# Kernel optimization log

Hardware: AMD Instinct MI355X
Metric: run time of the kernel (lower is better)

The kernel has to match this reference:

```python
import jax, jax.numpy as jnp
import numpy as np

H = 512

def _lstm_cell(x, h, c, Wih, Whh, bih, bhh):
    # PyTorch LSTMCell: gates ordered i, f, g, o
    g = x @ Wih.T + bih + h @ Whh.T + bhh
    i, f, gg, o = jnp.split(g, 4, axis=-1)
    i = jax.nn.sigmoid(i)
    f = jax.nn.sigmoid(f)
    gg = jnp.tanh(gg)
    o = jax.nn.sigmoid(o)
    c_new = f * c + i * gg
    h_new = o * jnp.tanh(c_new)
    return h_new, c_new


def setup_inputs() -> dict:
    key = jax.random.key(0)
    ks = jax.random.split(key, 12)
    B, T = 16, 6574
    s1 = 1.0 / np.sqrt(H)
    u = lambda k, shape: jax.random.uniform(k, shape, jnp.float32, -s1, s1)
    return {
        "input": jax.random.normal(ks[0], (B, T, 2), jnp.float32),
        "W_ih1": u(ks[1], (4 * H, 2)),
        "W_hh1": u(ks[2], (4 * H, H)),
        "b_ih1": u(ks[3], (4 * H,)),
        "b_hh1": u(ks[4], (4 * H,)),
        "W_ih2": u(ks[5], (4 * H, H)),
        "W_hh2": u(ks[6], (4 * H, H)),
        "b_ih2": u(ks[7], (4 * H,)),
        "b_hh2": u(ks[8], (4 * H,)),
        "W_out": u(ks[9], (1, H)),
        "b_out": u(ks[10], (1,)),
    }


def reference(input, W_ih1, W_hh1, b_ih1, b_hh1, W_ih2, W_hh2, b_ih2, b_hh2, W_out, b_out):
    B = input.shape[0]
    h1 = jnp.zeros((B, H), input.dtype)
    c1 = jnp.zeros((B, H), input.dtype)
    h2 = jnp.zeros((B, H), input.dtype)
    c2 = jnp.zeros((B, H), input.dtype)

    def step(carry, x_t):
        h1, c1, h2, c2 = carry
        h1, c1 = _lstm_cell(x_t, h1, c1, W_ih1, W_hh1, b_ih1, b_hh1)
        h2, c2 = _lstm_cell(h1, h2, c2, W_ih2, W_hh2, b_ih2, b_hh2)
        out_t = h2 @ W_out.T + b_out  # [B, 1]
        return (h1, c1, h2, c2), out_t

    xs = jnp.swapaxes(input, 0, 1)  # [T, B, 2]
    _, outs = jax.lax.scan(step, (h1, c1, h2, c2), xs)
    return jnp.swapaxes(outs, 0, 1)  # [B, T, 1]
```

## Files before the change

kernel.cpp:

```cpp
#include <hip/hip_runtime.h>
#include <math.h>

#define NWG  256
#define NTHR 256
#define AGT __HIP_MEMORY_SCOPE_AGENT

#define O_W2  0
#define O_W1  16384
#define O_U   24576
#define O_WX  33280
#define O_B1  33312
#define O_B2  33328
#define O_WO  33344
#define O_XS  33348
#define O_G1  33364
#define O_G2  33492
#define O_C1  33620
#define O_C2  33652
#define O_HN  33684
#define LDS_FLOATS 33720

union U64F2 { unsigned long long u; float f[2]; };

__global__ void ws_init_kernel(unsigned* flags, float* h1g, float* h2g) {
    int i = blockIdx.x * blockDim.x + threadIdx.x;
    int n = gridDim.x * blockDim.x;
    for (int j = i; j < NWG; j += n) flags[j] = 0u;
    for (int j = i; j < 16384; j += n) { h1g[j] = 0.0f; h2g[j] = 0.0f; }
}

__device__ __forceinline__ float sigm(float x) { return 1.0f / (1.0f + __expf(-x)); }
__device__ __forceinline__ float tanh_fast(float x) { return 2.0f / (1.0f + __expf(-2.0f * x)) - 1.0f; }

__device__ __forceinline__ void gbar(unsigned* flags, int wg, int tid, unsigned ph) {
    __syncthreads();
    asm volatile("s_waitcnt vmcnt(0)" ::: "memory");
    if (tid == 0)
        __hip_atomic_store(&flags[wg], ph, __ATOMIC_RELAXED, AGT);
    if (tid < 64) {
        const unsigned long long* f64 = (const unsigned long long*)flags;
        bool done;
        do {
            unsigned long long v0 = __hip_atomic_load(&f64[tid],      __ATOMIC_RELAXED, AGT);
            unsigned long long v1 = __hip_atomic_load(&f64[tid + 64], __ATOMIC_RELAXED, AGT);
            done = ((unsigned)v0 >= ph) && ((unsigned)(v0 >> 32) >= ph) &&
                   ((unsigned)v1 >= ph) && ((unsigned)(v1 >> 32) >= ph);
            if (!__all(done)) __builtin_amdgcn_s_sleep(2);
        } while (!__all(done));
    }
    __syncthreads();
}

__global__ __launch_bounds__(NTHR, 1) void lstm_kernel(
    const float* __restrict__ xin,  const float* __restrict__ Wih1,
    const float* __restrict__ Whh1, const float* __restrict__ bih1,
    const float* __restrict__ bhh1, const float* __restrict__ Wih2,
    const float* __restrict__ Whh2, const float* __restrict__ bih2,
    const float* __restrict__ bhh2, const float* __restrict__ Wout,
    const float* __restrict__ bout, float* __restrict__ out,
    unsigned* __restrict__ flags, float* __restrict__ h1g,
    float* __restrict__ h2g, float* __restrict__ outred, int T)
{
    __shared__ float lds[LDS_FLOATS];
    const int tid = threadIdx.x;
    const int wg  = blockIdx.x;
    const int bh  = wg & 1;
    const int jg  = wg >> 1;
    const int j0  = jg * 4;

    for (int idx = tid; idx < 2048; idx += NTHR) {
        int r = idx >> 7, c4 = idx & 127;
        int grow = (r >> 2) * 512 + j0 + (r & 3);
        *(float4*)&lds[O_W1 + r * 512 + c4 * 4] = *(const float4*)&Whh1[grow * 512 + c4 * 4];
    }
    for (int idx = tid; idx < 4096; idx += NTHR) {
        int r = idx >> 8, c4 = idx & 255;
        int grow = (r >> 2) * 512 + j0 + (r & 3);
        int k = c4 * 4;
        const float* src = (k < 512) ? &Wih2[grow * 512 + k] : &Whh2[grow * 512 + (k - 512)];
        *(float4*)&lds[O_W2 + r * 1024 + k] = *(const float4*)src;
    }
    if (tid < 32) {
        int r = tid >> 1, grow = (r >> 2) * 512 + j0 + (r & 3);
        lds[O_WX + tid] = Wih1[grow * 2 + (tid & 1)];
    }
    if (tid < 16) {
        int grow = (tid >> 2) * 512 + j0 + (tid & 3);
        lds[O_B1 + tid] = bih1[grow] + bhh1[grow];
        lds[O_B2 + tid] = bih2[grow] + bhh2[grow];
    }
    if (tid < 4) lds[O_WO + tid] = Wout[j0 + tid];
    if (tid < 32) { lds[O_C1 + tid] = 0.0f; lds[O_C2 + tid] = 0.0f; }
    const float bo = bout[0];
    __syncthreads();

    const int wv = tid >> 6;
    const int ks = tid & 63;
    unsigned ph = 0;

    for (int s = 0; s <= T; ++s) {
        const int p = s & 1, pq = p ^ 1;

        if (wg < 16 && s >= 2 && tid < 64) {
            const unsigned long long* row64 =
                (const unsigned long long*)(outred + pq * 2048 + wg * 128);
            U64F2 v; v.u = __hip_atomic_load(&row64[tid], __ATOMIC_RELAXED, AGT);
            float sum = v.f[0] + v.f[1];
            #pragma unroll
            for (int off = 32; off >= 1; off >>= 1) sum += __shfl_xor(sum, off);
            if (tid == 0) out[wg * T + (s - 2)] = sum + bo;
        }

        {
            const unsigned long long* h1s = (const unsigned long long*)(h1g + pq * 8192);
            const unsigned long long* h2s = (const unsigned long long*)(h2g + pq * 8192);
            unsigned long long tmp[16];
            #pragma unroll
            for (int i = 0; i < 16; ++i) {
                int idx = tid + i * NTHR;
                int b = idx >> 9, pos = idx & 511;
                tmp[i] = (pos < 256)
                    ? __hip_atomic_load(&h1s[(bh * 8 + b) * 256 + pos],         __ATOMIC_RELAXED, AGT)
                    : __hip_atomic_load(&h2s[(bh * 8 + b) * 256 + (pos - 256)], __ATOMIC_RELAXED, AGT);
            }
            #pragma unroll
            for (int i = 0; i < 16; ++i) {
                int idx = tid + i * NTHR;
                int b = idx >> 9, pos = idx & 511;
                *(unsigned long long*)&lds[O_U + b * 1024 + pos * 2] = tmp[i];
            }
        }
        if (tid < 16 && s < T) {
            int b = tid >> 1, cm = tid & 1;
            lds[O_XS + tid] = xin[((bh * 8 + b) * (long)T + s) * 2 + cm];
        }
        __syncthreads();

        float a1[4][8], a2[4][8];
        #pragma unroll
        for (int r = 0; r < 4; ++r)
            #pragma unroll
            for (int b = 0; b < 8; ++b) { a1[r][b] = 0.0f; a2[r][b] = 0.0f; }
        {
            const float* W2b = &lds[O_W2 + wv * 4096];
            const float* W1b = &lds[O_W1 + wv * 2048];
            #pragma unroll
            for (int c = 0; c < 4; ++c) {
                const int k = ks * 4 + c * 256;
                float4 u0 = *(const float4*)&W2b[k];
                float4 u1 = *(const float4*)&W2b[1024 + k];
                float4 u2 = *(const float4*)&W2b[2048 + k];
                float4 u3 = *(const float4*)&W2b[3072 + k];
                float4 w0, w1, w2, w3;
                if (c < 2) {
                    w0 = *(const float4*)&W1b[k];
                    w1 = *(const float4*)&W1b[512 + k];
                    w2 = *(const float4*)&W1b[1024 + k];
                    w3 = *(const float4*)&W1b[1536 + k];
                }
                #pragma unroll
                for (int b = 0; b < 8; ++b) {
                    float4 h = *(const float4*)&lds[O_U + b * 1024 + k];
                    a2[0][b] = fmaf(u0.x,h.x,fmaf(u0.y,h.y,fmaf(u0.z,h.z,fmaf(u0.w,h.w,a2[0][b]))));
                    a2[1][b] = fmaf(u1.x,h.x,fmaf(u1.y,h.y,fmaf(u1.z,h.z,fmaf(u1.w,h.w,a2[1][b]))));
                    a2[2][b] = fmaf(u2.x,h.x,fmaf(u2.y,h.y,fmaf(u2.z,h.z,fmaf(u2.w,h.w,a2[2][b]))));
                    a2[3][b] = fmaf(u3.x,h.x,fmaf(u3.y,h.y,fmaf(u3.z,h.z,fmaf(u3.w,h.w,a2[3][b]))));
                    if (c < 2) {
                        a1[0][b] = fmaf(w0.x,h.x,fmaf(w0.y,h.y,fmaf(w0.z,h.z,fmaf(w0.w,h.w,a1[0][b]))));
                        a1[1][b] = fmaf(w1.x,h.x,fmaf(w1.y,h.y,fmaf(w1.z,h.z,fmaf(w1.w,h.w,a1[1][b]))));
                        a1[2][b] = fmaf(w2.x,h.x,fmaf(w2.y,h.y,fmaf(w2.z,h.z,fmaf(w2.w,h.w,a1[2][b]))));
                        a1[3][b] = fmaf(w3.x,h.x,fmaf(w3.y,h.y,fmaf(w3.z,h.z,fmaf(w3.w,h.w,a1[3][b]))));
                    }
                }
            }
        }
        __syncthreads();

        #pragma unroll
        for (int r = 0; r < 4; ++r)
            #pragma unroll
            for (int b = 0; b < 8; ++b)
                lds[O_U + ((wv * 4 + r) * 8 + b) * 68 + ks] = a1[r][b];
        __syncthreads();
        {
            int o = tid >> 1, hf = tid & 1;
            const float* rr = &lds[O_U + o * 68 + hf * 32];
            float sum = 0.0f;
            #pragma unroll
            for (int c = 0; c < 8; ++c) { float4 v = *(const float4*)&rr[c * 4]; sum += v.x + v.y + v.z + v.w; }
            sum += __shfl_xor(sum, 1);
            if (hf == 0) {
                int r = o >> 3, b = o & 7;
                lds[O_G1 + o] = sum + lds[O_B1 + r]
                              + lds[O_WX + r * 2]     * lds[O_XS + b * 2]
                              + lds[O_WX + r * 2 + 1] * lds[O_XS + b * 2 + 1];
            }
        }
        __syncthreads();

        #pragma unroll
        for (int r = 0; r < 4; ++r)
            #pragma unroll
            for (int b = 0; b < 8; ++b)
                lds[O_U + ((wv * 4 + r) * 8 + b) * 68 + ks] = a2[r][b];
        __syncthreads();
        {
            int o = tid >> 1, hf = tid & 1;
            const float* rr = &lds[O_U + o * 68 + hf * 32];
            float sum = 0.0f;
            #pragma unroll
            for (int c = 0; c < 8; ++c) { float4 v = *(const float4*)&rr[c * 4]; sum += v.x + v.y + v.z + v.w; }
            sum += __shfl_xor(sum, 1);
            if (hf == 0) lds[O_G2 + o] = sum + lds[O_B2 + (o >> 3)];
        }
        __syncthreads();

        if (tid < 32) {
            if (s < T) {
                int jj = tid >> 3, b = tid & 7;
                float gi = sigm(lds[O_G1 + (0 * 4 + jj) * 8 + b]);
                float gf = sigm(lds[O_G1 + (1 * 4 + jj) * 8 + b]);
                float gg = tanh_fast(lds[O_G1 + (2 * 4 + jj) * 8 + b]);
                float go = sigm(lds[O_G1 + (3 * 4 + jj) * 8 + b]);
                float c  = gf * lds[O_C1 + tid] + gi * gg;
                lds[O_C1 + tid] = c;
                __hip_atomic_store(&h1g[p * 8192 + (bh * 8 + b) * 512 + j0 + jj],
                                   go * tanh_fast(c), __ATOMIC_RELAXED, AGT);
            }
        } else if (tid < 64) {
            if (s >= 1) {
                int t2 = tid - 32, jj = t2 >> 3, b = t2 & 7;
                float gi = sigm(lds[O_G2 + (0 * 4 + jj) * 8 + b]);
                float gf = sigm(lds[O_G2 + (1 * 4 + jj) * 8 + b]);
                float gg = tanh_fast(lds[O_G2 + (2 * 4 + jj) * 8 + b]);
                float go = sigm(lds[O_G2 + (3 * 4 + jj) * 8 + b]);
                float c  = gf * lds[O_C2 + t2] + gi * gg;
                lds[O_C2 + t2] = c;
                float h = go * tanh_fast(c);
                __hip_atomic_store(&h2g[p * 8192 + (bh * 8 + b) * 512 + j0 + jj],
                                   h, __ATOMIC_RELAXED, AGT);
                lds[O_HN + t2] = lds[O_WO + jj] * h;
            }
        }
        __syncthreads();
        if (tid < 8 && s >= 1) {
            float pr = lds[O_HN + tid] + lds[O_HN + 8 + tid]
                     + lds[O_HN + 16 + tid] + lds[O_HN + 24 + tid];
            __hip_atomic_store(&outred[p * 2048 + (bh * 8 + tid) * 128 + jg],
                               pr, __ATOMIC_RELAXED, AGT);
        }

        gbar(flags, wg, tid, ++ph);
    }

    if (wg < 16 && tid < 64) {
        const unsigned long long* row64 =
            (const unsigned long long*)(outred + (T & 1) * 2048 + wg * 128);
        U64F2 v; v.u = __hip_atomic_load(&row64[tid], __ATOMIC_RELAXED, AGT);
        float sum = v.f[0] + v.f[1];
        #pragma unroll
        for (int off = 32; off >= 1; off >>= 1) sum += __shfl_xor(sum, off);
        if (tid == 0) out[wg * T + (T - 1)] = sum + bo;
    }
}

extern "C" void kernel_launch(void* const* d_in, const int* in_sizes, int n_in,
                              void* d_out, int out_size, void* d_ws, size_t ws_size,
                              hipStream_t stream) {
    const float* xin  = (const float*)d_in[0];
    const float* Wih1 = (const float*)d_in[1];
    const float* Whh1 = (const float*)d_in[2];
    const float* bih1 = (const float*)d_in[3];
    const float* bhh1 = (const float*)d_in[4];
    const float* Wih2 = (const float*)d_in[5];
    const float* Whh2 = (const float*)d_in[6];
    const float* bih2 = (const float*)d_in[7];
    const float* bhh2 = (const float*)d_in[8];
    const float* Wout = (const float*)d_in[9];
    const float* bout = (const float*)d_in[10];
    float* outp = (float*)d_out;
    int T = in_sizes[0] / 32;

    unsigned* flags = (unsigned*)d_ws;
    float* h1g    = (float*)d_ws + 4096;
    float* h2g    = h1g + 16384;
    float* outredp= h2g + 16384;

    hipLaunchKernelGGL(ws_init_kernel, dim3(32), dim3(256), 0, stream, flags, h1g, h2g);

    hipLaunchKernelGGL(lstm_kernel, dim3(NWG), dim3(NTHR), 0, stream,
                       xin, Wih1, Whh1, bih1, bhh1, Wih2, Whh2, bih2, bhh2,
                       Wout, bout, outp, flags, h1g, h2g, outredp, T);
}
```

Baseline: 66.10 ms.

## Split grid barrier per batch half and distribute output reduction via atomics

The global barrier now synchronizes only the 128 workgroups that share the same batch half, so each group polls fewer flags and does not wait on unrelated workgroups. The final output reduction is spread across all workgroups: each adds a partial sum with atomicAdd into an output that an init kernel pre-fills with the bias. This removes a 64-lane reduction concentrated in 16 workgroups and is meant to shorten the per-step critical path. The cost is nondeterministic float summation order and extra atomic traffic.

```diff
diff --git a/kernel.cpp b/kernel.cpp
--- a/kernel.cpp
+++ b/kernel.cpp
@@ -22,11 +22,14 @@
 
 union U64F2 { unsigned long long u; float f[2]; };
 
-__global__ void ws_init_kernel(unsigned* flags, float* h1g, float* h2g) {
+__global__ void ws_init_kernel(unsigned* flags, float* h1g, float* h2g,
+                               float* out, const float* bout, int n_out) {
     int i = blockIdx.x * blockDim.x + threadIdx.x;
     int n = gridDim.x * blockDim.x;
+    float bo = bout[0];
     for (int j = i; j < NWG; j += n) flags[j] = 0u;
     for (int j = i; j < 16384; j += n) { h1g[j] = 0.0f; h2g[j] = 0.0f; }
+    for (int j = i; j < n_out; j += n) out[j] = bo;
 }
 
 __device__ __forceinline__ float sigm(float x) { return 1.0f / (1.0f + __expf(-x)); }
@@ -35,14 +38,15 @@
 __device__ __forceinline__ void gbar(unsigned* flags, int wg, int tid, unsigned ph) {
     __syncthreads();
     asm volatile("s_waitcnt vmcnt(0)" ::: "memory");
+    const int half = wg & 1;
     if (tid == 0)
-        __hip_atomic_store(&flags[wg], ph, __ATOMIC_RELAXED, AGT);
-    if (tid < 64) {
-        const unsigned long long* f64 = (const unsigned long long*)flags;
+        __hip_atomic_store(&flags[(half << 7) + (wg >> 1)], ph, __ATOMIC_RELAXED, AGT);
+    if (tid < 32) {
+        const unsigned long long* f64 = (const unsigned long long*)flags + (half << 6);
         bool done;
         do {
-            unsigned long long v0 = __hip_atomic_load(&f64[tid],      __ATOMIC_RELAXED, AGT);
-            unsigned long long v1 = __hip_atomic_load(&f64[tid + 64], __ATOMIC_RELAXED, AGT);
+            unsigned long long v0 = __hip_atomic_load(&f64[2 * tid],     __ATOMIC_RELAXED, AGT);
+            unsigned long long v1 = __hip_atomic_load(&f64[2 * tid + 1], __ATOMIC_RELAXED, AGT);
             done = ((unsigned)v0 >= ph) && ((unsigned)(v0 >> 32) >= ph) &&
                    ((unsigned)v1 >= ph) && ((unsigned)(v1 >> 32) >= ph);
             if (!__all(done)) __builtin_amdgcn_s_sleep(2);
@@ -67,6 +71,8 @@
     const int bh  = wg & 1;
     const int jg  = wg >> 1;
     const int j0  = jg * 4;
+    const int bd  = bh * 8 + (jg & 7);
+    const int jh  = jg >> 3;
 
     for (int idx = tid; idx < 2048; idx += NTHR) {
         int r = idx >> 7, c4 = idx & 127;
@@ -91,7 +97,6 @@
     }
     if (tid < 4) lds[O_WO + tid] = Wout[j0 + tid];
     if (tid < 32) { lds[O_C1 + tid] = 0.0f; lds[O_C2 + tid] = 0.0f; }
-    const float bo = bout[0];
     __syncthreads();
 
     const int wv = tid >> 6;
@@ -101,14 +106,16 @@
     for (int s = 0; s <= T; ++s) {
         const int p = s & 1, pq = p ^ 1;
 
-        if (wg < 16 && s >= 2 && tid < 64) {
+        if (s >= 2 && tid == 0) {
             const unsigned long long* row64 =
-                (const unsigned long long*)(outred + pq * 2048 + wg * 128);
-            U64F2 v; v.u = __hip_atomic_load(&row64[tid], __ATOMIC_RELAXED, AGT);
-            float sum = v.f[0] + v.f[1];
-            #pragma unroll
-            for (int off = 32; off >= 1; off >>= 1) sum += __shfl_xor(sum, off);
-            if (tid == 0) out[wg * T + (s - 2)] = sum + bo;
+                (const unsigned long long*)(outred + pq * 2048 + bd * 128 + jh * 8);
+            U64F2 v0; v0.u = __hip_atomic_load(&row64[0], __ATOMIC_RELAXED, AGT);
+            U64F2 v1; v1.u = __hip_atomic_load(&row64[1], __ATOMIC_RELAXED, AGT);
+            U64F2 v2; v2.u = __hip_atomic_load(&row64[2], __ATOMIC_RELAXED, AGT);
+            U64F2 v3; v3.u = __hip_atomic_load(&row64[3], __ATOMIC_RELAXED, AGT);
+            float sum = (v0.f[0] + v0.f[1]) + (v1.f[0] + v1.f[1])
+                      + (v2.f[0] + v2.f[1]) + (v3.f[0] + v3.f[1]);
+            atomicAdd(&out[bd * T + (s - 2)], sum);
         }
 
         {
@@ -253,14 +260,16 @@
         gbar(flags, wg, tid, ++ph);
     }
 
-    if (wg < 16 && tid < 64) {
+    if (tid == 0) {
         const unsigned long long* row64 =
-            (const unsigned long long*)(outred + (T & 1) * 2048 + wg * 128);
-        U64F2 v; v.u = __hip_atomic_load(&row64[tid], __ATOMIC_RELAXED, AGT);
-        float sum = v.f[0] + v.f[1];
-        #pragma unroll
-        for (int off = 32; off >= 1; off >>= 1) sum += __shfl_xor(sum, off);
-        if (tid == 0) out[wg * T + (T - 1)] = sum + bo;
+            (const unsigned long long*)(outred + (T & 1) * 2048 + bd * 128 + jh * 8);
+        U64F2 v0; v0.u = __hip_atomic_load(&row64[0], __ATOMIC_RELAXED, AGT);
+        U64F2 v1; v1.u = __hip_atomic_load(&row64[1], __ATOMIC_RELAXED, AGT);
+        U64F2 v2; v2.u = __hip_atomic_load(&row64[2], __ATOMIC_RELAXED, AGT);
+        U64F2 v3; v3.u = __hip_atomic_load(&row64[3], __ATOMIC_RELAXED, AGT);
+        float sum = (v0.f[0] + v0.f[1]) + (v1.f[0] + v1.f[1])
+                  + (v2.f[0] + v2.f[1]) + (v3.f[0] + v3.f[1]);
+        atomicAdd(&out[bd * T + (T - 1)], sum);
     }
 }
 
@@ -286,7 +295,8 @@
     float* h2g    = h1g + 16384;
     float* outredp= h2g + 16384;
 
-    hipLaunchKernelGGL(ws_init_kernel, dim3(32), dim3(256), 0, stream, flags, h1g, h2g);
+    hipLaunchKernelGGL(ws_init_kernel, dim3(64), dim3(256), 0, stream,
+                       flags, h1g, h2g, outp, bout, out_size);
 
     hipLaunchKernelGGL(lstm_kernel, dim3(NWG), dim3(NTHR), 0, stream,
                        xin, Wih1, Whh1, bih1, bhh1, Wih2, Whh2, bih2, bhh2,
```

Result: faster. 63.21 ms (-4.4%).
